# Performance work log

Hardware: AMD Instinct MI355X
Metric: run time of the kernel (lower is better)

Reference implementation:

```python
import jax, jax.numpy as jnp
import numpy as np

D_MODEL = 1024
N_HEAD = 8      # KV heads
N_QUERY = 4     # query groups per KV head
D_HEAD = D_MODEL // (N_HEAD * N_QUERY)  # 32
KV_DIM = D_HEAD * N_HEAD                # 256
BATCH, SEQ = 4, 1024
BASE = 10000.0


def _rope(x):
    """Interleaved RoPE as in the torch module. theta denominator is always
    d_model/2 = 512 (layer-level), even when applied to the 256-dim key."""
    d = x.shape[-1]
    d2 = d // 2
    dm2 = D_MODEL // 2
    theta = BASE ** (-jnp.arange(dm2, dtype=jnp.float32) / dm2)  # [512]
    pos = jnp.arange(x.shape[-2], dtype=jnp.float32)
    ang = pos[:, None] * theta[None, :d2]  # [S, d2]
    cos, sin = jnp.cos(ang), jnp.sin(ang)
    xe, xo = x[..., ::2], x[..., 1::2]
    out = jnp.stack([xe * cos - xo * sin, xo * cos + xe * sin], axis=-1)
    return out.reshape(x.shape)


def setup_inputs() -> dict:
    key = jax.random.key(0)
    ks = jax.random.split(key, 6)
    x = jax.random.normal(ks[0], (BATCH, SEQ, D_MODEL), dtype=jnp.float32)
    s = 0.02
    Wq = jax.random.normal(ks[1], (D_MODEL, D_MODEL), dtype=jnp.float32) * s
    Wk = jax.random.normal(ks[2], (KV_DIM, D_MODEL), dtype=jnp.float32) * s
    Wv = jax.random.normal(ks[3], (KV_DIM, D_MODEL), dtype=jnp.float32) * s
    Wo = jax.random.normal(ks[4], (D_MODEL, D_MODEL), dtype=jnp.float32) * s
    bo = jnp.zeros((D_MODEL,), dtype=jnp.float32)
    # causal mask: True = masked out
    causal = jnp.triu(jnp.ones((SEQ, SEQ), dtype=bool), k=1)
    mask = jnp.broadcast_to(causal[None, None], (BATCH, 1, SEQ, SEQ))
    return {"x": x, "Wq": Wq, "Wk": Wk, "Wv": Wv, "Wo": Wo, "bo": bo, "mask": mask}


def reference(x, Wq, Wk, Wv, Wo, bo, mask):
    n_b, n_seq, _ = x.shape
    q = _rope(x @ Wq.T)                 # [B,S,1024]
    k = _rope(x @ Wk.T)                 # [B,S,256]
    v = x @ Wv.T                        # [B,S,256]
    # head split; KV heads repeat-interleaved n_query times to match query heads
    qh = q.reshape(n_b, n_seq, N_QUERY * N_HEAD, D_HEAD).transpose(0, 2, 1, 3)
    kh = jnp.repeat(k.reshape(n_b, n_seq, N_HEAD, D_HEAD), N_QUERY, axis=2).transpose(0, 2, 1, 3)
    vh = jnp.repeat(v.reshape(n_b, n_seq, N_HEAD, D_HEAD), N_QUERY, axis=2).transpose(0, 2, 1, 3)
    scale = 1.0 / jnp.sqrt(jnp.float32(D_HEAD))
    scores = jnp.einsum('bhqd,bhkd->bhqk', qh, kh) * scale
    scores = jnp.where(mask, jnp.float32(-1e9), scores)
    probs = jax.nn.softmax(scores, axis=-1)
    probs = jnp.where(mask, jnp.float32(0.0), probs)
    out = jnp.einsum('bhqk,bhkd->bqhd', probs, vh)  # [B,S,32,32]
    out = out.reshape(n_b, n_seq, D_MODEL)
    return out @ Wo.T + bo
```

## Files before the change

kernel.cpp:

```cpp
#include <hip/hip_runtime.h>
#include <hip/hip_bf16.h>

typedef __attribute__((ext_vector_type(8))) short short8;
typedef __attribute__((ext_vector_type(4))) short short4v;
typedef __attribute__((ext_vector_type(4))) float float4v;

#define DEV __device__ __forceinline__

constexpr int SEQ = 1024;
constexpr int DM  = 1024;
constexpr int KVD = 256;
constexpr int MTOK = 4096;

constexpr float QSCALE = 0.25503487660444f;


DEV void load_lds16(const void* g, void* l) {
  __builtin_amdgcn_global_load_lds(
      (const __attribute__((address_space(1))) unsigned int*)g,
      (__attribute__((address_space(3))) unsigned int*)l, 16, 0, 0);
}

DEV unsigned short f2bf(float f) {
  unsigned int u = __float_as_uint(f);
  u += 0x7fffu + ((u >> 16) & 1u);
  return (unsigned short)(u >> 16);
}

DEV float fexp2(float x) {
  float y;
  asm("v_exp_f32 %0, %1" : "=v"(y) : "v"(x));
  return y;
}

DEV unsigned int cvtpk(float lo, float hi) {
  unsigned int r;
  asm("v_cvt_pk_bf16_f32 %0, %1, %2" : "=v"(r) : "v"(lo), "v"(hi));
  return r;
}

#if __has_builtin(__builtin_amdgcn_mfma_f32_16x16x16bf16_1k)
DEV float4v mfma16(short4v a, short4v b, float4v c) {
  return __builtin_amdgcn_mfma_f32_16x16x16bf16_1k(a, b, c, 0, 0, 0);
}
#else
DEV float4v mfma16(short4v a, short4v b, float4v c) {
  asm("v_mfma_f32_16x16x16_bf16 %0, %1, %2, %0" : "+v"(c) : "v"(a), "v"(b));
  return c;
}
#endif

#define WAIT_VM(N)  asm volatile("s_waitcnt vmcnt(" #N ")" ::: "memory")
#define WAIT_LG(N)  asm volatile("s_waitcnt lgkmcnt(" #N ")" ::: "memory")
#define WAIT_LGKM0  asm volatile("s_waitcnt lgkmcnt(0)" ::: "memory")
#define SBAR0       __builtin_amdgcn_sched_barrier(0)


__global__ __launch_bounds__(256)
void prep_kernel(const float* __restrict__ x,  const float* __restrict__ Wq,
                 const float* __restrict__ Wk, const float* __restrict__ Wv,
                 const float* __restrict__ Wo,
                 unsigned short* __restrict__ xb, unsigned short* __restrict__ Wqkvb,
                 unsigned short* __restrict__ Wob,
                 float* __restrict__ rc, float* __restrict__ rs)
{
  const int NX  = (MTOK*DM)/4;
  const int NWQ = (DM*DM)/4;
  const int NWK = (KVD*DM)/4;
  const int NCONV = NX + NWQ + 2*NWK + NWQ;
  int id = blockIdx.x*256 + threadIdx.x;
  if (id < NCONV) {
    const float* src; unsigned short* dst; int u;
    if      (id < NX)            { src = x;  dst = xb;                     u = id; }
    else if (id < NX+NWQ)        { src = Wq; dst = Wqkvb;                  u = id-NX; }
    else if (id < NX+NWQ+NWK)    { src = Wk; dst = Wqkvb + DM*DM;          u = id-(NX+NWQ); }
    else if (id < NX+NWQ+2*NWK)  { src = Wv; dst = Wqkvb + DM*DM+KVD*DM;   u = id-(NX+NWQ+NWK); }
    else                         { src = Wo; dst = Wob;                    u = id-(NX+NWQ+2*NWK); }
    float4 v = ((const float4*)src)[u];
    ushort4 o;
    o.x = f2bf(v.x); o.y = f2bf(v.y); o.z = f2bf(v.z); o.w = f2bf(v.w);
    ((ushort4*)dst)[u] = o;
  } else {
    int id2 = id - NCONV;
    if (id2 < SEQ*512) {
      int pos = id2 >> 9, i = id2 & 511;
      float theta = exp2f((float)i * (-13.287712379549449f/512.0f));
      float ang = (float)pos * theta;
      float sv, cv; sincosf(ang, &sv, &cv);
      rc[id2] = cv; rs[id2] = sv;
    }
  }
}


template<int MODE, int GY>
__global__ __launch_bounds__(256)
void gemm_nt(const unsigned short* __restrict__ A, const unsigned short* __restrict__ Bw,
             unsigned short* __restrict__ outQ, unsigned short* __restrict__ outK,
             unsigned short* __restrict__ outVt, float* __restrict__ outF,
             const float* __restrict__ bias,
             const float* __restrict__ rc, const float* __restrict__ rs)
{
  __shared__ __align__(16) unsigned short As[2][128*64];
  __shared__ __align__(16) unsigned short Bs[2][64*64];
  const int tid = threadIdx.x;
  const int w  = tid >> 6, l = tid & 63;
  const int lg = l >> 4, ll = l & 15;
  const int wr = w >> 1, wc = w & 1;

  const int bid = (int)blockIdx.x;
  const int f   = (bid & 7) * (4*GY) + (bid >> 3);
  const int brow = (f / GY) * 128, bcol = (f % GY) * 64;

  float4v acc[4][2];
#pragma unroll
  for (int i = 0; i < 4; ++i)
#pragma unroll
    for (int j = 0; j < 2; ++j) acc[i][j] = (float4v){0.f,0.f,0.f,0.f};

  auto stage = [&](int kt, int cur) {
#pragma unroll
    for (int blk = 0; blk < 4; ++blk) {
      int cid = blk*256 + w*64 + l;
      int row = cid >> 3, c = cid & 7;
      int cg = c ^ (row & 7);
      load_lds16(A + (size_t)(brow+row)*DM + kt*64 + cg*8,
                 &As[cur][(blk*256 + w*64)*8]);
    }
#pragma unroll
    for (int blk = 0; blk < 2; ++blk) {
      int cid = blk*256 + w*64 + l;
      int row = cid >> 3, c = cid & 7;
      int cg = c ^ (row & 7);
      load_lds16(Bw + (size_t)(bcol+row)*DM + kt*64 + cg*8,
                 &Bs[cur][(blk*256 + w*64)*8]);
    }
  };

  stage(0, 0); stage(1, 1);
#pragma unroll 1
  for (int kt = 0; kt < 16; ++kt) {
    const int cur = kt & 1;
    if (kt < 15) { WAIT_VM(6); }
    else         { WAIT_VM(0); }
    __builtin_amdgcn_s_barrier();

    short8 af[2][4], bf[2][2];
#pragma unroll
    for (int mi = 0; mi < 4; ++mi) {
      int row = wr*64 + mi*16 + ll;
      af[0][mi] = *(const short8*)&As[cur][row*64 + ((lg ^ (row & 7)) << 3)];
    }
#pragma unroll
    for (int ni = 0; ni < 2; ++ni) {
      int col = wc*32 + ni*16 + ll;
      bf[0][ni] = *(const short8*)&Bs[cur][col*64 + ((lg ^ (col & 7)) << 3)];
    }
    SBAR0;
#pragma unroll
    for (int mi = 0; mi < 4; ++mi) {
      int row = wr*64 + mi*16 + ll;
      af[1][mi] = *(const short8*)&As[cur][row*64 + (((4 + lg) ^ (row & 7)) << 3)];
    }
#pragma unroll
    for (int ni = 0; ni < 2; ++ni) {
      int col = wc*32 + ni*16 + ll;
      bf[1][ni] = *(const short8*)&Bs[cur][col*64 + (((4 + lg) ^ (col & 7)) << 3)];
    }
    WAIT_LG(6);
    SBAR0;
    __builtin_amdgcn_s_setprio(1);
#pragma unroll
    for (int mi = 0; mi < 4; ++mi)
#pragma unroll
      for (int ni = 0; ni < 2; ++ni)
        acc[mi][ni] = __builtin_amdgcn_mfma_f32_16x16x32_bf16(af[0][mi], bf[0][ni], acc[mi][ni], 0,0,0);
    __builtin_amdgcn_s_setprio(0);
    SBAR0;
    WAIT_LGKM0;
    SBAR0;
    __builtin_amdgcn_s_barrier();

    if (kt + 2 < 16) stage(kt + 2, cur);

    __builtin_amdgcn_s_setprio(1);
#pragma unroll
    for (int mi = 0; mi < 4; ++mi)
#pragma unroll
      for (int ni = 0; ni < 2; ++ni)
        acc[mi][ni] = __builtin_amdgcn_mfma_f32_16x16x32_bf16(af[1][mi], bf[1][ni], acc[mi][ni], 0,0,0);
    __builtin_amdgcn_s_setprio(0);
  }

#pragma unroll
  for (int mi = 0; mi < 4; ++mi)
#pragma unroll
    for (int ni = 0; ni < 2; ++ni)
#pragma unroll
      for (int r = 0; r < 4; ++r) {
        int m = brow + wr*64 + mi*16 + lg*4 + r;
        int n = bcol + wc*32 + ni*16 + ll;
        float v = acc[mi][ni][r];
        if constexpr (MODE == 0) {
          float p = __shfl_xor(v, 1);
          if (n < DM) {
            int pos = m & (SEQ-1);
            int i = n >> 1;
            float ct = rc[pos*512 + i], st = rs[pos*512 + i];
            v = (n & 1) ? (v*ct + p*st) : (v*ct - p*st);
            outQ[(size_t)m*DM + n] = f2bf(v * QSCALE);
          } else if (n < DM + KVD) {
            int nk = n - DM;
            int pos = m & (SEQ-1);
            int i = nk >> 1;
            float ct = rc[pos*512 + i], st = rs[pos*512 + i];
            v = (nk & 1) ? (v*ct + p*st) : (v*ct - p*st);
            outK[(size_t)m*KVD + nk] = f2bf(v);
          } else {
            int nv = n - DM - KVD;
            outVt[((size_t)(m >> 10)*KVD + nv)*SEQ + (m & (SEQ-1))] = f2bf(v);
          }
        } else {
          outF[(size_t)m*DM + n] = v + bias[n];
        }
      }
}


__global__ __launch_bounds__(256)
void attn_kernel(const unsigned short* __restrict__ Qb, const unsigned short* __restrict__ Kb,
                 const unsigned short* __restrict__ Vtb, unsigned short* __restrict__ Ob)
{
  __shared__ __align__(16) unsigned short Kl[3][128*32];
  __shared__ __align__(16) unsigned short Vl[3][32*128];
  const int tid = threadIdx.x;
  const int w  = tid >> 6, l = tid & 63;
  const int lg = l >> 4, ll = l & 15;
  const int hk = blockIdx.y, b = blockIdx.z;
  const int h  = hk*4 + w;

  auto stage = [&](int kvt, int bi) {
    const int kv0 = kvt*128;
#pragma unroll
    for (int blk = 0; blk < 2; ++blk) {
      int cid = blk*256 + tid;
      int row = cid >> 2, c = cid & 3, cl = c ^ ((row >> 1) & 3);
      load_lds16(&Kb[((size_t)b*SEQ + kv0 + row)*KVD + hk*32 + cl*8],
                 &Kl[bi][(blk*256 + w*64)*8]);
    }
#pragma unroll
    for (int blk = 0; blk < 2; ++blk) {
      int cid = blk*256 + tid;
      int d = cid >> 4, c = cid & 15, cl = c ^ (d & 7);
      load_lds16(&Vtb[((size_t)b*KVD + hk*32 + d)*SEQ + kv0 + cl*8],
                 &Vl[bi][(blk*256 + w*64)*8]);
    }
  };

#pragma unroll 1
  for (int ph = 0; ph < 2; ++ph) {
    const int qt = ph ? (int)blockIdx.x : 31 - (int)blockIdx.x;
    const int nt = (qt + 4) >> 2;
    const int q0 = qt*32;

    short8 qf[2];
#pragma unroll
    for (int qi = 0; qi < 2; ++qi)
      qf[qi] = *(const short8*)&Qb[((size_t)b*SEQ + q0 + qi*16 + ll)*DM + h*32 + (lg<<3)];

    float4v o[2][2];
    float mrow[2] = {-1e30f, -1e30f};
    float lrow[2] = {0.f, 0.f};
#pragma unroll
    for (int qi = 0; qi < 2; ++qi)
#pragma unroll
      for (int df = 0; df < 2; ++df) o[qi][df] = (float4v){0,0,0,0};

    WAIT_VM(0);
    stage(0, 0);
    if (1 < nt) stage(1, 1);
    if (2 < nt) stage(2, 2);

    int bi = 0;
    for (int kvt = 0; kvt < nt; ++kvt) {
      if (kvt + 3 <= nt)      { WAIT_VM(8); }
      else if (kvt + 2 == nt) { WAIT_VM(4); }
      else                    { WAIT_VM(0); }
      __builtin_amdgcn_s_barrier();

      short8 kf[8];
#pragma unroll
      for (int ni = 0; ni < 8; ++ni) {
        int kv = ni*16 + ll;
        kf[ni] = *(const short8*)&Kl[bi][kv*32 + ((lg ^ ((ll >> 1) & 3)) << 3)];
      }
      short4v vf[2][8];
#pragma unroll
      for (int df = 0; df < 2; ++df) {
        int d = df*16 + ll;
#pragma unroll
        for (int ni = 0; ni < 8; ++ni) {
          int ch = (ni*2 + (lg >> 1)) ^ (ll & 7);
          vf[df][ni] = *(const short4v*)&Vl[bi][d*128 + (ch << 3) + ((lg & 1) << 2)];
        }
      }
      WAIT_LGKM0;
      __builtin_amdgcn_sched_barrier(0);
      __builtin_amdgcn_s_barrier();

      if (kvt + 3 < nt) stage(kvt + 3, bi);

      const bool lastTile = (kvt == nt-1);
#pragma unroll
      for (int qi = 0; qi < 2; ++qi) {
        float sc[8][4];
        __builtin_amdgcn_s_setprio(1);
#pragma unroll
        for (int ni = 0; ni < 8; ++ni) {
          float4v s = __builtin_amdgcn_mfma_f32_16x16x32_bf16(kf[ni], qf[qi],
                         (float4v){0,0,0,0}, 0,0,0);
#pragma unroll
          for (int r = 0; r < 4; ++r) sc[ni][r] = s[r];
        }
        __builtin_amdgcn_s_setprio(0);

        if (lastTile) {
          int q = q0 + qi*16 + ll;
#pragma unroll
          for (int ni = 0; ni < 8; ++ni)
#pragma unroll
            for (int r = 0; r < 4; ++r) {
              int kv = kvt*128 + ni*16 + lg*4 + r;
              if (kv > q) sc[ni][r] = -1e30f;
            }
        }

        float mt = fmaxf(fmaxf(sc[0][0], sc[0][1]), fmaxf(sc[0][2], sc[0][3]));
#pragma unroll
        for (int ni = 1; ni < 8; ++ni)
          mt = fmaxf(mt, fmaxf(fmaxf(sc[ni][0], sc[ni][1]), fmaxf(sc[ni][2], sc[ni][3])));
        mt = fmaxf(mt, __shfl_xor(mt, 16));
        mt = fmaxf(mt, __shfl_xor(mt, 32));

        const bool grow = !__all(mt <= mrow[qi]);
        float mn = grow ? fmaxf(mrow[qi], mt) : mrow[qi];
        float s0 = 0.f;
        short4v pf[8];
#pragma unroll
        for (int ni = 0; ni < 8; ++ni) {
          float p0 = fexp2(sc[ni][0] - mn);
          float p1 = fexp2(sc[ni][1] - mn);
          float p2 = fexp2(sc[ni][2] - mn);
          float p3 = fexp2(sc[ni][3] - mn);
          s0 += (p0 + p1) + (p2 + p3);
          unsigned int w0 = cvtpk(p0, p1), w1 = cvtpk(p2, p3);
          union { unsigned int u[2]; short4v s4; } cv;
          cv.u[0] = w0; cv.u[1] = w1;
          pf[ni] = cv.s4;
        }
        if (grow) {
          float corr = fexp2(mrow[qi] - mn);
          mrow[qi] = mn;
          lrow[qi] = lrow[qi]*corr + s0;
#pragma unroll
          for (int df = 0; df < 2; ++df)
#pragma unroll
            for (int r = 0; r < 4; ++r) o[qi][df][r] *= corr;
        } else {
          lrow[qi] += s0;
        }

        __builtin_amdgcn_s_setprio(1);
#pragma unroll
        for (int df = 0; df < 2; ++df)
#pragma unroll
          for (int ni = 0; ni < 8; ++ni)
            o[qi][df] = mfma16(vf[df][ni], pf[ni], o[qi][df]);
        __builtin_amdgcn_s_setprio(0);
      }

      bi = (bi == 2) ? 0 : bi + 1;
    }

#pragma unroll
    for (int qi = 0; qi < 2; ++qi) {
      float s = lrow[qi];
      s += __shfl_xor(s, 16);
      s += __shfl_xor(s, 32);
      float inv = 1.f / s;
      size_t tok = (size_t)b*SEQ + q0 + qi*16 + ll;
#pragma unroll
      for (int df = 0; df < 2; ++df) {
        short4v sv;
#pragma unroll
        for (int r = 0; r < 4; ++r) sv[r] = (short)f2bf(o[qi][df][r] * inv);
        *(short4v*)&Ob[tok*DM + h*32 + df*16 + lg*4] = sv;
      }
    }
  }
}


extern "C" void kernel_launch(void* const* d_in, const int* in_sizes, int n_in,
                              void* d_out, int out_size, void* d_ws, size_t ws_size,
                              hipStream_t stream)
{
  const float* x  = (const float*)d_in[0];
  const float* Wq = (const float*)d_in[1];
  const float* Wk = (const float*)d_in[2];
  const float* Wv = (const float*)d_in[3];
  const float* Wo = (const float*)d_in[4];
  const float* bo = (const float*)d_in[5];
  float* out = (float*)d_out;

  char* ws = (char*)d_ws;
  const size_t MB = 1u << 20;
  unsigned short* xb    = (unsigned short*)(ws + 0*MB);
  unsigned short* Wqkvb = (unsigned short*)(ws + 8*MB);
  unsigned short* Wob   = (unsigned short*)(ws + 11*MB);
  float*          rc    = (float*)(ws + 13*MB);
  float*          rs    = (float*)(ws + 15*MB);
  unsigned short* Qb    = (unsigned short*)(ws + 17*MB);
  unsigned short* Kb    = (unsigned short*)(ws + 25*MB);
  unsigned short* Vt    = (unsigned short*)(ws + 27*MB);
  unsigned short* Ob    = (unsigned short*)(ws + 29*MB);
  if (ws_size < 37*MB) return;

  {
    const int total = 1703936 + SEQ*512;
    const int blocks = (total + 255) / 256;
    prep_kernel<<<blocks, 256, 0, stream>>>(x, Wq, Wk, Wv, Wo, xb, Wqkvb, Wob, rc, rs);
  }
  gemm_nt<0, 24><<<dim3(768), 256, 0, stream>>>(xb, Wqkvb, Qb, Kb, Vt, nullptr, nullptr, rc, rs);
  attn_kernel<<<dim3(16, 8, 4), 256, 0, stream>>>(Qb, Kb, Vt, Ob);
  gemm_nt<2, 16><<<dim3(512), 256, 0, stream>>>(Ob, Wob, nullptr, nullptr, nullptr, out, bo, rc, rs);
}
```

Before: 90.23 us.

## Halve attention query tile per block, double-buffer KV, double grid size

The attention kernel now processes 16 queries per wave per phase instead of 32, launching twice as many blocks. KV staging drops from triple to double buffering to cut LDS use, and launch bounds request 3 blocks per CU. The aim is higher occupancy and better load balance across CUs. The cost is that each K/V tile is loaded twice as often, and the shallower prefetch pipeline hides less latency.

```diff
diff --git a/kernel.cpp b/kernel.cpp
--- a/kernel.cpp
+++ b/kernel.cpp
@@ -227,12 +227,12 @@
 }
 
 
-__global__ __launch_bounds__(256)
+__global__ __launch_bounds__(256, 3)
 void attn_kernel(const unsigned short* __restrict__ Qb, const unsigned short* __restrict__ Kb,
                  const unsigned short* __restrict__ Vtb, unsigned short* __restrict__ Ob)
 {
-  __shared__ __align__(16) unsigned short Kl[3][128*32];
-  __shared__ __align__(16) unsigned short Vl[3][32*128];
+  __shared__ __align__(16) unsigned short Kl[2][128*32];
+  __shared__ __align__(16) unsigned short Vl[2][32*128];
   const int tid = threadIdx.x;
   const int w  = tid >> 6, l = tid & 63;
   const int lg = l >> 4, ll = l & 15;
@@ -259,33 +259,25 @@
 
 #pragma unroll 1
   for (int ph = 0; ph < 2; ++ph) {
-    const int qt = ph ? (int)blockIdx.x : 31 - (int)blockIdx.x;
-    const int nt = (qt + 4) >> 2;
-    const int q0 = qt*32;
-
-    short8 qf[2];
-#pragma unroll
-    for (int qi = 0; qi < 2; ++qi)
-      qf[qi] = *(const short8*)&Qb[((size_t)b*SEQ + q0 + qi*16 + ll)*DM + h*32 + (lg<<3)];
-
-    float4v o[2][2];
-    float mrow[2] = {-1e30f, -1e30f};
-    float lrow[2] = {0.f, 0.f};
-#pragma unroll
-    for (int qi = 0; qi < 2; ++qi)
-#pragma unroll
-      for (int df = 0; df < 2; ++df) o[qi][df] = (float4v){0,0,0,0};
+    const int qt = ph ? (int)blockIdx.x : 63 - (int)blockIdx.x;
+    const int nt = (qt + 8) >> 3;
+    const int q0 = qt*16;
+
+    short8 qf = *(const short8*)&Qb[((size_t)b*SEQ + q0 + ll)*DM + h*32 + (lg<<3)];
+
+    float4v o[2];
+    float mrow = -1e30f, lrow = 0.f;
+    o[0] = (float4v){0,0,0,0}; o[1] = (float4v){0,0,0,0};
 
     WAIT_VM(0);
     stage(0, 0);
     if (1 < nt) stage(1, 1);
-    if (2 < nt) stage(2, 2);
-
-    int bi = 0;
+
+#pragma unroll 2
     for (int kvt = 0; kvt < nt; ++kvt) {
-      if (kvt + 3 <= nt)      { WAIT_VM(8); }
-      else if (kvt + 2 == nt) { WAIT_VM(4); }
-      else                    { WAIT_VM(0); }
+      const int bi = kvt & 1;
+      if (kvt + 1 < nt) { WAIT_VM(4); }
+      else              { WAIT_VM(0); }
       __builtin_amdgcn_s_barrier();
 
       short8 kf[8];
@@ -308,94 +300,85 @@
       __builtin_amdgcn_sched_barrier(0);
       __builtin_amdgcn_s_barrier();
 
-      if (kvt + 3 < nt) stage(kvt + 3, bi);
-
-      const bool lastTile = (kvt == nt-1);
-#pragma unroll
-      for (int qi = 0; qi < 2; ++qi) {
-        float sc[8][4];
-        __builtin_amdgcn_s_setprio(1);
-#pragma unroll
-        for (int ni = 0; ni < 8; ++ni) {
-          float4v s = __builtin_amdgcn_mfma_f32_16x16x32_bf16(kf[ni], qf[qi],
-                         (float4v){0,0,0,0}, 0,0,0);
-#pragma unroll
-          for (int r = 0; r < 4; ++r) sc[ni][r] = s[r];
-        }
-        __builtin_amdgcn_s_setprio(0);
-
-        if (lastTile) {
-          int q = q0 + qi*16 + ll;
-#pragma unroll
-          for (int ni = 0; ni < 8; ++ni)
-#pragma unroll
-            for (int r = 0; r < 4; ++r) {
-              int kv = kvt*128 + ni*16 + lg*4 + r;
-              if (kv > q) sc[ni][r] = -1e30f;
-            }
-        }
-
-        float mt = fmaxf(fmaxf(sc[0][0], sc[0][1]), fmaxf(sc[0][2], sc[0][3]));
-#pragma unroll
-        for (int ni = 1; ni < 8; ++ni)
-          mt = fmaxf(mt, fmaxf(fmaxf(sc[ni][0], sc[ni][1]), fmaxf(sc[ni][2], sc[ni][3])));
-        mt = fmaxf(mt, __shfl_xor(mt, 16));
-        mt = fmaxf(mt, __shfl_xor(mt, 32));
-
-        const bool grow = !__all(mt <= mrow[qi]);
-        float mn = grow ? fmaxf(mrow[qi], mt) : mrow[qi];
-        float s0 = 0.f;
-        short4v pf[8];
-#pragma unroll
-        for (int ni = 0; ni < 8; ++ni) {
-          float p0 = fexp2(sc[ni][0] - mn);
-          float p1 = fexp2(sc[ni][1] - mn);
-          float p2 = fexp2(sc[ni][2] - mn);
-          float p3 = fexp2(sc[ni][3] - mn);
-          s0 += (p0 + p1) + (p2 + p3);
-          unsigned int w0 = cvtpk(p0, p1), w1 = cvtpk(p2, p3);
-          union { unsigned int u[2]; short4v s4; } cv;
-          cv.u[0] = w0; cv.u[1] = w1;
-          pf[ni] = cv.s4;
-        }
-        if (grow) {
-          float corr = fexp2(mrow[qi] - mn);
-          mrow[qi] = mn;
-          lrow[qi] = lrow[qi]*corr + s0;
-#pragma unroll
-          for (int df = 0; df < 2; ++df)
-#pragma unroll
-            for (int r = 0; r < 4; ++r) o[qi][df][r] *= corr;
-        } else {
-          lrow[qi] += s0;
-        }
-
-        __builtin_amdgcn_s_setprio(1);
+      if (kvt + 2 < nt) stage(kvt + 2, bi);
+
+      float sc[8][4];
+      __builtin_amdgcn_s_setprio(1);
+#pragma unroll
+      for (int ni = 0; ni < 8; ++ni) {
+        float4v s = __builtin_amdgcn_mfma_f32_16x16x32_bf16(kf[ni], qf,
+                       (float4v){0,0,0,0}, 0,0,0);
+#pragma unroll
+        for (int r = 0; r < 4; ++r) sc[ni][r] = s[r];
+      }
+      __builtin_amdgcn_s_setprio(0);
+
+      if (kvt == nt-1) {
+        int q = q0 + ll;
+#pragma unroll
+        for (int ni = 0; ni < 8; ++ni)
+#pragma unroll
+          for (int r = 0; r < 4; ++r) {
+            int kv = kvt*128 + ni*16 + lg*4 + r;
+            if (kv > q) sc[ni][r] = -1e30f;
+          }
+      }
+
+      float mt = fmaxf(fmaxf(sc[0][0], sc[0][1]), fmaxf(sc[0][2], sc[0][3]));
+#pragma unroll
+      for (int ni = 1; ni < 8; ++ni)
+        mt = fmaxf(mt, fmaxf(fmaxf(sc[ni][0], sc[ni][1]), fmaxf(sc[ni][2], sc[ni][3])));
+      mt = fmaxf(mt, __shfl_xor(mt, 16));
+      mt = fmaxf(mt, __shfl_xor(mt, 32));
+
+      const bool grow = !__all(mt <= mrow);
+      float mn = grow ? fmaxf(mrow, mt) : mrow;
+      float s0 = 0.f;
+      short4v pf[8];
+#pragma unroll
+      for (int ni = 0; ni < 8; ++ni) {
+        float p0 = fexp2(sc[ni][0] - mn);
+        float p1 = fexp2(sc[ni][1] - mn);
+        float p2 = fexp2(sc[ni][2] - mn);
+        float p3 = fexp2(sc[ni][3] - mn);
+        s0 += (p0 + p1) + (p2 + p3);
+        unsigned int w0 = cvtpk(p0, p1), w1 = cvtpk(p2, p3);
+        union { unsigned int u[2]; short4v s4; } cv;
+        cv.u[0] = w0; cv.u[1] = w1;
+        pf[ni] = cv.s4;
+      }
+      if (grow) {
+        float corr = fexp2(mrow - mn);
+        mrow = mn;
+        lrow = lrow*corr + s0;
 #pragma unroll
         for (int df = 0; df < 2; ++df)
 #pragma unroll
-          for (int ni = 0; ni < 8; ++ni)
-            o[qi][df] = mfma16(vf[df][ni], pf[ni], o[qi][df]);
-        __builtin_amdgcn_s_setprio(0);
-      }
-
-      bi = (bi == 2) ? 0 : bi + 1;
-    }
-
-#pragma unroll
-    for (int qi = 0; qi < 2; ++qi) {
-      float s = lrow[qi];
-      s += __shfl_xor(s, 16);
-      s += __shfl_xor(s, 32);
-      float inv = 1.f / s;
-      size_t tok = (size_t)b*SEQ + q0 + qi*16 + ll;
-#pragma unroll
-      for (int df = 0; df < 2; ++df) {
-        short4v sv;
-#pragma unroll
-        for (int r = 0; r < 4; ++r) sv[r] = (short)f2bf(o[qi][df][r] * inv);
-        *(short4v*)&Ob[tok*DM + h*32 + df*16 + lg*4] = sv;
-      }
+          for (int r = 0; r < 4; ++r) o[df][r] *= corr;
+      } else {
+        lrow += s0;
+      }
+
+      __builtin_amdgcn_s_setprio(1);
+#pragma unroll
+      for (int df = 0; df < 2; ++df)
+#pragma unroll
+        for (int ni = 0; ni < 8; ++ni)
+          o[df] = mfma16(vf[df][ni], pf[ni], o[df]);
+      __builtin_amdgcn_s_setprio(0);
+    }
+
+    float s = lrow;
+    s += __shfl_xor(s, 16);
+    s += __shfl_xor(s, 32);
+    float inv = 1.f / s;
+    size_t tok = (size_t)b*SEQ + q0 + ll;
+#pragma unroll
+    for (int df = 0; df < 2; ++df) {
+      short4v sv;
+#pragma unroll
+      for (int r = 0; r < 4; ++r) sv[r] = (short)f2bf(o[df][r] * inv);
+      *(short4v*)&Ob[tok*DM + h*32 + df*16 + lg*4] = sv;
     }
   }
 }
@@ -432,6 +415,6 @@
     prep_kernel<<<blocks, 256, 0, stream>>>(x, Wq, Wk, Wv, Wo, xb, Wqkvb, Wob, rc, rs);
   }
   gemm_nt<0, 24><<<dim3(768), 256, 0, stream>>>(xb, Wqkvb, Qb, Kb, Vt, nullptr, nullptr, rc, rs);
-  attn_kernel<<<dim3(16, 8, 4), 256, 0, stream>>>(Qb, Kb, Vt, Ob);
+  attn_kernel<<<dim3(32, 8, 4), 256, 0, stream>>>(Qb, Kb, Vt, Ob);
   gemm_nt<2, 16><<<dim3(512), 256, 0, stream>>>(Ob, Wob, nullptr, nullptr, nullptr, out, bo, rc, rs);
 }
```

Result: faster. 87.43 us (-3.1%).
